# Kernel optimization log

Hardware: AMD Instinct MI355X
Metric: run time of the kernel (lower is better)

Reference implementation:

```python
import jax, jax.numpy as jnp
import numpy as np

DIM = 1024
NUM_HEADS = 16
HEAD_DIM = DIM // NUM_HEADS
SCALE = HEAD_DIM ** -0.5


def setup_inputs() -> dict:
    key = jax.random.key(0)
    k1, k2, k3 = jax.random.split(key, 3)
    x = jax.random.normal(k1, (4, 2048, DIM), dtype=jnp.float32)
    w_qkv = jax.random.normal(k2, (DIM, 3 * DIM), dtype=jnp.float32) * (DIM ** -0.5)
    b_qkv = jnp.zeros((3 * DIM,), dtype=jnp.float32)
    w_proj = jax.random.normal(k3, (DIM, DIM), dtype=jnp.float32) * (DIM ** -0.5)
    b_proj = jnp.zeros((DIM,), dtype=jnp.float32)
    return {"x": x, "w_qkv": w_qkv, "b_qkv": b_qkv, "w_proj": w_proj, "b_proj": b_proj}


def reference(x, w_qkv, b_qkv, w_proj, b_proj):
    b, n, c = x.shape
    qkv = x @ w_qkv + b_qkv                       # [b, n, 3*dim]
    qkv = qkv.reshape(b, n, 3, NUM_HEADS, HEAD_DIM)
    qkv = jnp.transpose(qkv, (2, 0, 3, 1, 4))     # [3, b, H, n, hd]
    q, k, v = qkv[0], qkv[1], qkv[2]
    attn = jnp.einsum("bhqd,bhkd->bhqk", q, k) * SCALE
    attn = jax.nn.softmax(attn, axis=-1)
    out = jnp.einsum("bhqk,bhkd->bhqd", attn, v)  # [b, H, n, hd]
    out = jnp.transpose(out, (0, 2, 1, 3)).reshape(b, n, c)
    return out @ w_proj + b_proj
```

## Files before the change

### kernel.cpp

```cpp
#include <hip/hip_runtime.h>
#include <hip/hip_bf16.h>

typedef unsigned short u16;
typedef __attribute__((ext_vector_type(8))) short bf16x8;
typedef __attribute__((ext_vector_type(4))) float f32x4;
typedef __attribute__((ext_vector_type(16))) float f32x16;


__device__ __forceinline__ u16 f2bf(float f) {
  union { float f; unsigned u; } v; v.f = f;
  unsigned r = v.u + 0x7fffu + ((v.u >> 16) & 1u);
  return (u16)(r >> 16);
}

#if defined(__has_builtin)
#if __has_builtin(__builtin_amdgcn_cvt_pk_bf16_f32)
#define HAS_PK_BF16 1
#endif
#endif
__device__ __forceinline__ unsigned pk2bf(float a, float b) {
#ifdef HAS_PK_BF16
  typedef __attribute__((ext_vector_type(2))) __bf16 vbf2;
  union { vbf2 v; unsigned u; } u;
  u.v = __builtin_amdgcn_cvt_pk_bf16_f32(a, b);
  return u.u;
#else
  return (unsigned)f2bf(a) | ((unsigned)f2bf(b) << 16);
#endif
}

__device__ __forceinline__ f32x4 mfma16(bf16x8 a, bf16x8 b, f32x4 c) {
  return __builtin_amdgcn_mfma_f32_16x16x32_bf16(a, b, c, 0, 0, 0);
}
__device__ __forceinline__ f32x16 mfma32(bf16x8 a, bf16x8 b, f32x16 c) {
  return __builtin_amdgcn_mfma_f32_32x32x16_bf16(a, b, c, 0, 0, 0);
}

__device__ __forceinline__ void gl_lds16(const void* g, void* l) {
  __builtin_amdgcn_global_load_lds((__attribute__((address_space(1))) void*)g,
                                   (__attribute__((address_space(3))) void*)l,
                                   16, 0, 0);
}

__device__ __forceinline__ void stage128x32(const u16* g0, int ld, u16* lds) {
  const int t = threadIdx.x;
  const int wave = t >> 6;
#pragma unroll
  for (int j = 0; j < 2; ++j) {
    int c = j * 256 + t;
    const u16* gp = g0 + (size_t)(c >> 2) * ld + (c & 3) * 8;
    gl_lds16(gp, lds + (size_t)(j * 256 + wave * 64) * 8);
  }
}


__global__ void cvt_f32_bf16(const float* __restrict__ in, u16* __restrict__ out, int n) {
  int i = (blockIdx.x * blockDim.x + threadIdx.x) * 4;
  if (i >= n) return;
  float4 v = *(const float4*)(in + i);
  u16 o0 = f2bf(v.x), o1 = f2bf(v.y), o2 = f2bf(v.z), o3 = f2bf(v.w);
  ushort4 o; o.x = o0; o.y = o1; o.z = o2; o.w = o3;
  *(ushort4*)(out + i) = o;
}

__global__ void transpose_cvt(const float* __restrict__ in, u16* __restrict__ out,
                              int R, int C) {
  __shared__ u16 tile[64][65];
  int c0 = blockIdx.x * 64, r0 = blockIdx.y * 64;
  int lc = threadIdx.x & 63, lr = threadIdx.x >> 6;
#pragma unroll
  for (int i = 0; i < 16; ++i) {
    int r = lr + i * 4;
    tile[r][lc] = f2bf(in[(size_t)(r0 + r) * C + c0 + lc]);
  }
  __syncthreads();
#pragma unroll
  for (int i = 0; i < 16; ++i) {
    int c = lr + i * 4;
    out[(size_t)(c0 + c) * R + r0 + lc] = tile[lc][c];
  }
}

__global__ void transpose_v(const u16* __restrict__ Vb, u16* __restrict__ Vt) {
  __shared__ u16 tile[64][65];
  int bh = blockIdx.y;
  int s0 = blockIdx.x * 64;
  const u16* in = Vb + (size_t)bh * 2048 * 64;
  u16* out = Vt + (size_t)bh * 64 * 2048;
  int lc = threadIdx.x & 63, lr = threadIdx.x >> 6;
#pragma unroll
  for (int i = 0; i < 16; ++i) {
    int r = lr + i * 4;
    tile[r][lc] = in[(size_t)(s0 + r) * 64 + lc];
  }
  __syncthreads();
#pragma unroll
  for (int i = 0; i < 16; ++i) {
    int d = lr + i * 4;
    out[(size_t)d * 2048 + s0 + lc] = tile[lc][d];
  }
}


__global__ __launch_bounds__(256, 2) void gemm_qkv(
    const u16* __restrict__ A, const u16* __restrict__ Bt,
    const float* __restrict__ bias,
    u16* __restrict__ Qb, u16* __restrict__ Kb, u16* __restrict__ Vb) {
  __shared__ u16 As[128 * 32], Bs[128 * 32];
  const int row0 = blockIdx.x * 128, col0 = blockIdx.y * 128;
  const int t = threadIdx.x, lane = t & 63, wave = t >> 6;
  const int quad = lane >> 4, l15 = lane & 15;
  const int m_off = (wave & 1) * 64, n_off = (wave >> 1) * 64;
  f32x4 acc[4][4] = {};
  for (int k0 = 0; k0 < 1024; k0 += 32) {
    __syncthreads();
    stage128x32(A + (size_t)row0 * 1024 + k0, 1024, As);
    stage128x32(Bt + (size_t)col0 * 1024 + k0, 1024, Bs);
    __syncthreads();
    bf16x8 a[4], b[4];
#pragma unroll
    for (int mi = 0; mi < 4; ++mi)
      a[mi] = *(const bf16x8*)(As + (m_off + mi * 16 + l15) * 32 + quad * 8);
#pragma unroll
    for (int ni = 0; ni < 4; ++ni)
      b[ni] = *(const bf16x8*)(Bs + (n_off + ni * 16 + l15) * 32 + quad * 8);
#pragma unroll
    for (int mi = 0; mi < 4; ++mi)
#pragma unroll
      for (int ni = 0; ni < 4; ++ni)
        acc[mi][ni] = mfma16(a[mi], b[ni], acc[mi][ni]);
  }
  const int which = col0 >> 10;
  u16* dst = which == 0 ? Qb : (which == 1 ? Kb : Vb);
  const float qscale = which == 0 ? 0.1803368801111137f : 1.0f;
#pragma unroll
  for (int ni = 0; ni < 4; ++ni) {
    int col = col0 + n_off + ni * 16 + l15;
    float bv = bias[col];
    int h = (col >> 6) & 15, d = col & 63;
#pragma unroll
    for (int mi = 0; mi < 4; ++mi) {
#pragma unroll
      for (int r = 0; r < 4; ++r) {
        int row = row0 + m_off + mi * 16 + quad * 4 + r;
        int bb = row >> 11, s = row & 2047;
        float v = (acc[mi][ni][r] + bv) * qscale;
        dst[(((size_t)bb * 16 + h) * 2048 + s) * 64 + d] = f2bf(v);
      }
    }
  }
}


__global__ __launch_bounds__(256, 2) void gemm_proj(
    const u16* __restrict__ A, const u16* __restrict__ Bt,
    const float* __restrict__ bias, float* __restrict__ C) {
  __shared__ u16 As[128 * 32], Bs[128 * 32];
  const int row0 = blockIdx.x * 128, col0 = blockIdx.y * 128;
  const int t = threadIdx.x, lane = t & 63, wave = t >> 6;
  const int quad = lane >> 4, l15 = lane & 15;
  const int m_off = (wave & 1) * 64, n_off = (wave >> 1) * 64;
  f32x4 acc[4][4] = {};
  for (int k0 = 0; k0 < 1024; k0 += 32) {
    __syncthreads();
    stage128x32(A + (size_t)row0 * 1024 + k0, 1024, As);
    stage128x32(Bt + (size_t)col0 * 1024 + k0, 1024, Bs);
    __syncthreads();
    bf16x8 a[4], b[4];
#pragma unroll
    for (int mi = 0; mi < 4; ++mi)
      a[mi] = *(const bf16x8*)(As + (m_off + mi * 16 + l15) * 32 + quad * 8);
#pragma unroll
    for (int ni = 0; ni < 4; ++ni)
      b[ni] = *(const bf16x8*)(Bs + (n_off + ni * 16 + l15) * 32 + quad * 8);
#pragma unroll
    for (int mi = 0; mi < 4; ++mi)
#pragma unroll
      for (int ni = 0; ni < 4; ++ni)
        acc[mi][ni] = mfma16(a[mi], b[ni], acc[mi][ni]);
  }
#pragma unroll
  for (int ni = 0; ni < 4; ++ni) {
    int col = col0 + n_off + ni * 16 + l15;
    float bv = bias[col];
#pragma unroll
    for (int mi = 0; mi < 4; ++mi) {
#pragma unroll
      for (int r = 0; r < 4; ++r) {
        int row = row0 + m_off + mi * 16 + quad * 4 + r;
        C[(size_t)row * 1024 + col] = acc[mi][ni][r] + bv;
      }
    }
  }
}


__device__ __forceinline__ void attn_tile(
    const u16* __restrict__ Ks, const u16* __restrict__ Vs,
    bf16x8 qf0, bf16x8 qf1, bf16x8 qf2, bf16x8 qf3,
    int l31, int hi, f32x16& acc0, f32x16& acc1, float& l_part) {
  f32x16 s0 = {}, s1 = {};
  const bf16x8 qf[4] = {qf0, qf1, qf2, qf3};
#pragma unroll
  for (int dc = 0; dc < 4; ++dc) {
    const int ch = dc * 2 + hi;
    {
      const int row = l31;
      bf16x8 kf = *(const bf16x8*)(Ks + ((size_t)row * 8 + (ch ^ (row & 7))) * 8);
      s0 = mfma32(kf, qf[dc], s0);
    }
    {
      const int row = 32 + l31;
      bf16x8 kf = *(const bf16x8*)(Ks + ((size_t)row * 8 + (ch ^ (row & 7))) * 8);
      s1 = mfma32(kf, qf[dc], s1);
    }
  }
  unsigned D[16];
  float l = 0.f;
#pragma unroll
  for (int i = 0; i < 8; ++i) {
    float a = __builtin_amdgcn_exp2f(s0[2 * i] - 24.f);
    float b = __builtin_amdgcn_exp2f(s0[2 * i + 1] - 24.f);
    l += a + b;
    D[i] = pk2bf(a, b);
  }
#pragma unroll
  for (int i = 0; i < 8; ++i) {
    float a = __builtin_amdgcn_exp2f(s1[2 * i] - 24.f);
    float b = __builtin_amdgcn_exp2f(s1[2 * i + 1] - 24.f);
    l += a + b;
    D[8 + i] = pk2bf(a, b);
  }
  l_part += l;
#pragma unroll
  for (int c = 0; c < 4; ++c) {
    unsigned x = D[4 * c], y = D[4 * c + 2];
    unsigned x2 = D[4 * c + 1], y2 = D[4 * c + 3];
    asm volatile("v_permlane32_swap_b32 %0, %1" : "+v"(x), "+v"(y));
    asm volatile("v_permlane32_swap_b32 %0, %1" : "+v"(x2), "+v"(y2));
    union { unsigned u[4]; bf16x8 v; } pa;
    pa.u[0] = x; pa.u[1] = x2; pa.u[2] = y; pa.u[3] = y2;
    const int ch = c * 2 + hi;
    {
      const int d = l31;
      bf16x8 vf = *(const bf16x8*)(Vs + ((size_t)d * 8 + (ch ^ (d & 7))) * 8);
      acc0 = mfma32(pa.v, vf, acc0);
    }
    {
      const int d = 32 + l31;
      bf16x8 vf = *(const bf16x8*)(Vs + ((size_t)d * 8 + (ch ^ (d & 7))) * 8);
      acc1 = mfma32(pa.v, vf, acc1);
    }
  }
}

__global__ __launch_bounds__(256, 3) void attn_kernel(
    const u16* __restrict__ Qb, const u16* __restrict__ Kb,
    const u16* __restrict__ Vt, u16* __restrict__ Ob) {
  __shared__ u16 KsA[64 * 64], KsB[64 * 64];
  __shared__ u16 VsA[64 * 64], VsB[64 * 64];
  const int bh = blockIdx.x, q0 = blockIdx.y * 128;
  const u16* Qp = Qb + (size_t)bh * 2048 * 64;
  const u16* Kp = Kb + (size_t)bh * 2048 * 64;
  const u16* Vp = Vt + (size_t)bh * 64 * 2048;
  const int t = threadIdx.x, lane = t & 63, wave = t >> 6;
  const int l31 = lane & 31, hi = lane >> 5;

  const int kr0 = t >> 3, kc0 = (t & 7) ^ (kr0 & 7);
  const int kr1 = (256 + t) >> 3, kc1 = ((256 + t) & 7) ^ (kr1 & 7);
  const u16* Kg0 = Kp + (size_t)kr0 * 64 + kc0 * 8;
  const u16* Kg1 = Kp + (size_t)kr1 * 64 + kc1 * 8;
  const u16* Vg0 = Vp + (size_t)kr0 * 2048 + kc0 * 8;
  const u16* Vg1 = Vp + (size_t)kr1 * 2048 + kc1 * 8;
  const size_t dof0 = (size_t)wave * 512;
  const size_t dof1 = 2048 + (size_t)wave * 512;

#define STAGE(Kd, Vd, key0)                                   \
  do {                                                        \
    gl_lds16(Kg0 + (size_t)(key0) * 64, (Kd) + dof0);         \
    gl_lds16(Kg1 + (size_t)(key0) * 64, (Kd) + dof1);         \
    gl_lds16(Vg0 + (key0), (Vd) + dof0);                      \
    gl_lds16(Vg1 + (key0), (Vd) + dof1);                      \
  } while (0)

  STAGE(KsA, VsA, 0);
  const u16* Qrow = Qp + (size_t)(q0 + wave * 32 + l31) * 64 + hi * 8;
  bf16x8 qf0 = *(const bf16x8*)(Qrow);
  bf16x8 qf1 = *(const bf16x8*)(Qrow + 16);
  bf16x8 qf2 = *(const bf16x8*)(Qrow + 32);
  bf16x8 qf3 = *(const bf16x8*)(Qrow + 48);
  __syncthreads();

  f32x16 acc0 = {}, acc1 = {};
  float l_part = 0.f;

#pragma unroll 1
  for (int kt2 = 0; kt2 < 16; ++kt2) {
    const int kt = kt2 * 2;
    STAGE(KsB, VsB, (kt + 1) * 64);
    attn_tile(KsA, VsA, qf0, qf1, qf2, qf3, l31, hi, acc0, acc1, l_part);
    __syncthreads();
    if (kt2 < 15) STAGE(KsA, VsA, (kt + 2) * 64);
    attn_tile(KsB, VsB, qf0, qf1, qf2, qf3, l31, hi, acc0, acc1, l_part);
    __syncthreads();
  }
#undef STAGE

  l_part += __shfl_xor(l_part, 32);
  float inv = 1.f / l_part;

  const int b_ = bh >> 4, h = bh & 15;
  const int qw = q0 + wave * 32;
#pragma unroll
  for (int r = 0; r < 16; ++r) {
    const int ql = (r & 3) + 8 * (r >> 2) + 4 * hi;
    float invr = __shfl(inv, ql);
    size_t base = ((size_t)b_ * 2048 + qw + ql) * 1024 + h * 64;
    Ob[base + l31] = f2bf(acc0[r] * invr);
    Ob[base + 32 + l31] = f2bf(acc1[r] * invr);
  }
}


extern "C" void kernel_launch(void* const* d_in, const int* in_sizes, int n_in,
                              void* d_out, int out_size, void* d_ws, size_t ws_size,
                              hipStream_t stream) {
  const float* x      = (const float*)d_in[0];
  const float* w_qkv  = (const float*)d_in[1];
  const float* b_qkv  = (const float*)d_in[2];
  const float* w_proj = (const float*)d_in[3];
  const float* b_proj = (const float*)d_in[4];
  float* out = (float*)d_out;
  char* ws = (char*)d_ws;

  u16* xb    = (u16*)(ws);
  u16* wqkvt = (u16*)(ws + 16777216);
  u16* wprjt = (u16*)(ws + 23068672);
  u16* Qb    = (u16*)(ws + 25165824);
  u16* Kb    = (u16*)(ws + 41943040);
  u16* Vb    = (u16*)(ws + 58720256);
  u16* Vt    = (u16*)(ws + 75497472);
  u16* Ob    = xb;
  if (ws_size < 92274688u) return;

  cvt_f32_bf16<<<8192, 256, 0, stream>>>(x, xb, 8388608);
  transpose_cvt<<<dim3(48, 16), 256, 0, stream>>>(w_qkv, wqkvt, 1024, 3072);
  transpose_cvt<<<dim3(16, 16), 256, 0, stream>>>(w_proj, wprjt, 1024, 1024);
  gemm_qkv<<<dim3(64, 24), 256, 0, stream>>>(xb, wqkvt, b_qkv, Qb, Kb, Vb);
  transpose_v<<<dim3(32, 64), 256, 0, stream>>>(Vb, Vt);
  attn_kernel<<<dim3(64, 16), 256, 0, stream>>>(Qb, Kb, Vt, Ob);
  gemm_proj<<<dim3(64, 8), 256, 0, stream>>>(Ob, wprjt, b_proj, out);
}
```

Before: 292.7 us.

## Process 64 queries per wave in attention to reuse K/V LDS fragments

Each wave of the attention kernel now covers two 32-query blocks (64 rows) instead of one. Every K and V fragment read from shared memory feeds twice as many MFMAs, which halves LDS traffic per unit of work and also halves the number of K/V global loads across the grid. The query tile per block grows to 256, so the grid shrinks to 512 blocks and launch bounds drop to 2 blocks per CU to make room for the larger register footprint (four 32x32 accumulators plus two sets of Q fragments). The constant -24 offset inside exp2 is also dropped; it cancels in the final normalisation, but removing it gives less headroom against fp32 overflow.

```diff
diff --git a/kernel.cpp b/kernel.cpp
--- a/kernel.cpp
+++ b/kernel.cpp
@@ -195,71 +195,40 @@
 }
 
 
-__device__ __forceinline__ void attn_tile(
-    const u16* __restrict__ Ks, const u16* __restrict__ Vs,
-    bf16x8 qf0, bf16x8 qf1, bf16x8 qf2, bf16x8 qf3,
-    int l31, int hi, f32x16& acc0, f32x16& acc1, float& l_part) {
-  f32x16 s0 = {}, s1 = {};
-  const bf16x8 qf[4] = {qf0, qf1, qf2, qf3};
-#pragma unroll
-  for (int dc = 0; dc < 4; ++dc) {
-    const int ch = dc * 2 + hi;
-    {
-      const int row = l31;
-      bf16x8 kf = *(const bf16x8*)(Ks + ((size_t)row * 8 + (ch ^ (row & 7))) * 8);
-      s0 = mfma32(kf, qf[dc], s0);
-    }
-    {
-      const int row = 32 + l31;
-      bf16x8 kf = *(const bf16x8*)(Ks + ((size_t)row * 8 + (ch ^ (row & 7))) * 8);
-      s1 = mfma32(kf, qf[dc], s1);
-    }
-  }
-  unsigned D[16];
-  float l = 0.f;
+__device__ __forceinline__ void softmax32(const f32x16& s, float& l,
+                                          bf16x8& paA, bf16x8& paB) {
+  unsigned D[8];
 #pragma unroll
   for (int i = 0; i < 8; ++i) {
-    float a = __builtin_amdgcn_exp2f(s0[2 * i] - 24.f);
-    float b = __builtin_amdgcn_exp2f(s0[2 * i + 1] - 24.f);
+    float a = __builtin_amdgcn_exp2f(s[2 * i]);
+    float b = __builtin_amdgcn_exp2f(s[2 * i + 1]);
     l += a + b;
     D[i] = pk2bf(a, b);
   }
-#pragma unroll
-  for (int i = 0; i < 8; ++i) {
-    float a = __builtin_amdgcn_exp2f(s1[2 * i] - 24.f);
-    float b = __builtin_amdgcn_exp2f(s1[2 * i + 1] - 24.f);
-    l += a + b;
-    D[8 + i] = pk2bf(a, b);
-  }
-  l_part += l;
-#pragma unroll
-  for (int c = 0; c < 4; ++c) {
-    unsigned x = D[4 * c], y = D[4 * c + 2];
-    unsigned x2 = D[4 * c + 1], y2 = D[4 * c + 3];
+  {
+    unsigned x = D[0], x2 = D[1], y = D[2], y2 = D[3];
     asm volatile("v_permlane32_swap_b32 %0, %1" : "+v"(x), "+v"(y));
     asm volatile("v_permlane32_swap_b32 %0, %1" : "+v"(x2), "+v"(y2));
-    union { unsigned u[4]; bf16x8 v; } pa;
-    pa.u[0] = x; pa.u[1] = x2; pa.u[2] = y; pa.u[3] = y2;
-    const int ch = c * 2 + hi;
-    {
-      const int d = l31;
-      bf16x8 vf = *(const bf16x8*)(Vs + ((size_t)d * 8 + (ch ^ (d & 7))) * 8);
-      acc0 = mfma32(pa.v, vf, acc0);
-    }
-    {
-      const int d = 32 + l31;
-      bf16x8 vf = *(const bf16x8*)(Vs + ((size_t)d * 8 + (ch ^ (d & 7))) * 8);
-      acc1 = mfma32(pa.v, vf, acc1);
-    }
-  }
-}
-
-__global__ __launch_bounds__(256, 3) void attn_kernel(
+    union { unsigned u[4]; bf16x8 v; } p;
+    p.u[0] = x; p.u[1] = x2; p.u[2] = y; p.u[3] = y2;
+    paA = p.v;
+  }
+  {
+    unsigned x = D[4], x2 = D[5], y = D[6], y2 = D[7];
+    asm volatile("v_permlane32_swap_b32 %0, %1" : "+v"(x), "+v"(y));
+    asm volatile("v_permlane32_swap_b32 %0, %1" : "+v"(x2), "+v"(y2));
+    union { unsigned u[4]; bf16x8 v; } p;
+    p.u[0] = x; p.u[1] = x2; p.u[2] = y; p.u[3] = y2;
+    paB = p.v;
+  }
+}
+
+__global__ __launch_bounds__(256, 2) void attn_kernel(
     const u16* __restrict__ Qb, const u16* __restrict__ Kb,
     const u16* __restrict__ Vt, u16* __restrict__ Ob) {
   __shared__ u16 KsA[64 * 64], KsB[64 * 64];
   __shared__ u16 VsA[64 * 64], VsB[64 * 64];
-  const int bh = blockIdx.x, q0 = blockIdx.y * 128;
+  const int bh = blockIdx.x, q0 = blockIdx.y * 256;
   const u16* Qp = Qb + (size_t)bh * 2048 * 64;
   const u16* Kp = Kb + (size_t)bh * 2048 * 64;
   const u16* Vp = Vt + (size_t)bh * 64 * 2048;
@@ -284,40 +253,86 @@
   } while (0)
 
   STAGE(KsA, VsA, 0);
-  const u16* Qrow = Qp + (size_t)(q0 + wave * 32 + l31) * 64 + hi * 8;
-  bf16x8 qf0 = *(const bf16x8*)(Qrow);
-  bf16x8 qf1 = *(const bf16x8*)(Qrow + 16);
-  bf16x8 qf2 = *(const bf16x8*)(Qrow + 32);
-  bf16x8 qf3 = *(const bf16x8*)(Qrow + 48);
+  const u16* Qr0 = Qp + (size_t)(q0 + wave * 64 + l31) * 64 + hi * 8;
+  const u16* Qr1 = Qr0 + 32 * 64;
+  bf16x8 qf0[4], qf1[4];
+#pragma unroll
+  for (int dc = 0; dc < 4; ++dc) {
+    qf0[dc] = *(const bf16x8*)(Qr0 + dc * 16);
+    qf1[dc] = *(const bf16x8*)(Qr1 + dc * 16);
+  }
   __syncthreads();
 
-  f32x16 acc0 = {}, acc1 = {};
-  float l_part = 0.f;
+  const int rm = l31 & 7;
+  int off[2][4];
+#pragma unroll
+  for (int x = 0; x < 2; ++x)
+#pragma unroll
+    for (int c = 0; c < 4; ++c)
+      off[x][c] = x * 4096 + l31 * 128 + (((c * 2 + hi) ^ rm) << 4);
+
+  f32x16 acc00 = {}, acc01 = {}, acc10 = {}, acc11 = {};
+  float l0 = 0.f, l1 = 0.f;
+
+#define TILE(Ks, Vs)                                                          \
+  do {                                                                        \
+    _Pragma("unroll")                                                         \
+    for (int kh = 0; kh < 2; ++kh) {                                          \
+      f32x16 s0 = {}, s1 = {};                                                \
+      _Pragma("unroll")                                                       \
+      for (int dc = 0; dc < 4; ++dc) {                                        \
+        bf16x8 kf = *(const bf16x8*)((const char*)(Ks) + off[kh][dc]);        \
+        s0 = mfma32(kf, qf0[dc], s0);                                         \
+        s1 = mfma32(kf, qf1[dc], s1);                                         \
+      }                                                                       \
+      bf16x8 pa00, pa01, pa10, pa11;                                          \
+      softmax32(s0, l0, pa00, pa01);                                          \
+      softmax32(s1, l1, pa10, pa11);                                          \
+      _Pragma("unroll")                                                       \
+      for (int ci = 0; ci < 2; ++ci) {                                        \
+        const int c = 2 * kh + ci;                                            \
+        bf16x8 vlo = *(const bf16x8*)((const char*)(Vs) + off[0][c]);         \
+        bf16x8 vhiv = *(const bf16x8*)((const char*)(Vs) + off[1][c]);        \
+        bf16x8 pa0 = ci ? pa01 : pa00;                                        \
+        bf16x8 pa1 = ci ? pa11 : pa10;                                        \
+        acc00 = mfma32(pa0, vlo, acc00);                                      \
+        acc01 = mfma32(pa0, vhiv, acc01);                                     \
+        acc10 = mfma32(pa1, vlo, acc10);                                      \
+        acc11 = mfma32(pa1, vhiv, acc11);                                     \
+      }                                                                       \
+    }                                                                         \
+  } while (0)
 
 #pragma unroll 1
   for (int kt2 = 0; kt2 < 16; ++kt2) {
     const int kt = kt2 * 2;
     STAGE(KsB, VsB, (kt + 1) * 64);
-    attn_tile(KsA, VsA, qf0, qf1, qf2, qf3, l31, hi, acc0, acc1, l_part);
+    TILE(KsA, VsA);
     __syncthreads();
     if (kt2 < 15) STAGE(KsA, VsA, (kt + 2) * 64);
-    attn_tile(KsB, VsB, qf0, qf1, qf2, qf3, l31, hi, acc0, acc1, l_part);
-    __syncthreads();
-  }
+    TILE(KsB, VsB);
+    __syncthreads();
+  }
+#undef TILE
 #undef STAGE
 
-  l_part += __shfl_xor(l_part, 32);
-  float inv = 1.f / l_part;
+  l0 += __shfl_xor(l0, 32);
+  l1 += __shfl_xor(l1, 32);
+  float inv0 = 1.f / l0, inv1 = 1.f / l1;
 
   const int b_ = bh >> 4, h = bh & 15;
-  const int qw = q0 + wave * 32;
+  const int qw = q0 + wave * 64;
 #pragma unroll
   for (int r = 0; r < 16; ++r) {
     const int ql = (r & 3) + 8 * (r >> 2) + 4 * hi;
-    float invr = __shfl(inv, ql);
-    size_t base = ((size_t)b_ * 2048 + qw + ql) * 1024 + h * 64;
-    Ob[base + l31] = f2bf(acc0[r] * invr);
-    Ob[base + 32 + l31] = f2bf(acc1[r] * invr);
+    float iv0 = __shfl(inv0, ql);
+    float iv1 = __shfl(inv1, ql);
+    size_t base0 = ((size_t)b_ * 2048 + qw + ql) * 1024 + h * 64;
+    size_t base1 = base0 + (size_t)32 * 1024;
+    Ob[base0 + l31] = f2bf(acc00[r] * iv0);
+    Ob[base0 + 32 + l31] = f2bf(acc01[r] * iv0);
+    Ob[base1 + l31] = f2bf(acc10[r] * iv1);
+    Ob[base1 + 32 + l31] = f2bf(acc11[r] * iv1);
   }
 }
 
@@ -348,6 +363,6 @@
   transpose_cvt<<<dim3(16, 16), 256, 0, stream>>>(w_proj, wprjt, 1024, 1024);
   gemm_qkv<<<dim3(64, 24), 256, 0, stream>>>(xb, wqkvt, b_qkv, Qb, Kb, Vb);
   transpose_v<<<dim3(32, 64), 256, 0, stream>>>(Vb, Vt);
-  attn_kernel<<<dim3(64, 16), 256, 0, stream>>>(Qb, Kb, Vt, Ob);
+  attn_kernel<<<dim3(64, 8), 256, 0, stream>>>(Qb, Kb, Vt, Ob);
   gemm_proj<<<dim3(64, 8), 256, 0, stream>>>(Ob, wprjt, b_proj, out);
 }
```

After: 278.8 us. -4.8%, faster.
